# Performance work log

Hardware: AMD Instinct MI355X
Metric: run time of the kernel (lower is better)

Reference implementation:

```python
import jax, jax.numpy as jnp
import numpy as np

B, N, E = 32, 128, 16384
NI, NH, NO, NA = 72, 72, 72, 8
C_WEIGHT = 1.0
EPS = 1e-5  # torch BatchNorm1d default eps


def _psi(p):
    return jnp.sign(p) * jnp.log1p(jnp.abs(p))


def _normsq4(p):
    psq = p * p
    return 2.0 * psq[..., 0] - psq.sum(axis=-1)


def _dotsq4(p, q):
    psq = p * q
    return 2.0 * psq[..., 0] - psq.sum(axis=-1)


def _bn_train(z, g, b):
    # BatchNorm1d in training mode over flattened rows (biased variance)
    mu = z.mean(axis=0)
    var = z.var(axis=0)
    return (z - mu) * jax.lax.rsqrt(var + EPS) * g + b


def _seg_sum(data, ids):
    # data: [B,E,D], ids: [B,E] -> [B,N,D]
    return jax.vmap(lambda d, i: jax.ops.segment_sum(d, i, num_segments=N))(data, ids)


def _init(k, fan_in, shape, scale=1.0):
    return jax.random.normal(k, shape, jnp.float32) * (scale / np.sqrt(fan_in))


def setup_inputs() -> dict:
    key = jax.random.key(0)
    ks = jax.random.split(key, 24)
    d_e_in = 2 * NI + 2
    d_h_in = NH + NI + NA
    return {
        "h": jax.random.normal(ks[0], (B, N, NI), jnp.float32),
        "x": jax.random.normal(ks[1], (B, N, 4), jnp.float32),
        "edgei": jax.random.randint(ks[2], (B, E), 0, N, jnp.int32),
        "edgej": jax.random.randint(ks[3], (B, E), 0, N, jnp.int32),
        "node_attr": jax.random.normal(ks[4], (B, N, NA), jnp.float32),
        # phi_e: Linear(no bias) -> BN -> ReLU -> Linear -> ReLU
        "W_e1": _init(ks[5], d_e_in, (d_e_in, NH)),
        "g_e": jnp.ones((NH,), jnp.float32),
        "be_e": jnp.zeros((NH,), jnp.float32),
        "W_e2": _init(ks[6], NH, (NH, NH)),
        "b_e2": jnp.zeros((NH,), jnp.float32),
        # phi_m: Linear -> Sigmoid
        "W_m": _init(ks[7], NH, (NH, 1)),
        "b_m": jnp.zeros((1,), jnp.float32),
        # phi_x: Linear -> ReLU -> Linear(no bias, tiny xavier gain 0.001)
        "W_x1": _init(ks[8], NH, (NH, NH)),
        "b_x1": jnp.zeros((NH,), jnp.float32),
        "W_x2": _init(ks[9], NH, (NH, 1), scale=0.001),
        # phi_h: Linear -> BN -> ReLU -> Linear
        "W_h1": _init(ks[10], d_h_in, (d_h_in, NH)),
        "b_h1": jnp.zeros((NH,), jnp.float32),
        "g_h": jnp.ones((NH,), jnp.float32),
        "be_h": jnp.zeros((NH,), jnp.float32),
        "W_h2": _init(ks[11], NH, (NH, NO)),
        "b_h2": jnp.zeros((NO,), jnp.float32),
    }


def reference(h, x, edgei, edgej, node_attr, W_e1, g_e, be_e, W_e2, b_e2,
              W_m, b_m, W_x1, b_x1, W_x2, W_h1, b_h1, g_h, be_h, W_h2, b_h2):
    ii = edgei[..., None]  # [B,E,1]
    jj = edgej[..., None]
    # minkowski_feats
    xi = jnp.take_along_axis(x, ii, axis=1)  # [B,E,4]
    xj = jnp.take_along_axis(x, jj, axis=1)
    x_diff = xi - xj
    norms = _psi(_normsq4(x_diff))[..., None]  # [B,E,1]
    dots = _psi(_dotsq4(xi, xj))[..., None]
    # m_model
    hi = jnp.take_along_axis(h, ii, axis=1)  # [B,E,NI]
    hj = jnp.take_along_axis(h, jj, axis=1)
    feat = jnp.concatenate([hi, hj, norms, dots], axis=-1).reshape(-1, 2 * NI + 2)
    z = jax.nn.relu(_bn_train(feat @ W_e1, g_e, be_e))
    z = jax.nn.relu(z @ W_e2 + b_e2)
    m_e = z.reshape(B, E, NH)
    w = jax.nn.sigmoid(m_e @ W_m + b_m)  # [B,E,1]
    m = m_e * w
    # x_model (not last_layer)
    phix = jax.nn.relu(m @ W_x1 + b_x1) @ W_x2  # [B,E,1]
    trans = jnp.clip(x_diff * phix, -100.0, 100.0)
    agg = _seg_sum(trans, edgei)
    cnt = _seg_sum(jnp.ones_like(trans), edgei)
    x_out = x + (agg / jnp.maximum(cnt, 1.0)) * C_WEIGHT
    # h_model
    magg = _seg_sum(m, edgei)  # [B,N,NH]
    cat = jnp.concatenate([h, magg, node_attr], axis=-1).reshape(-1, NH + NI + NA)
    zh = jax.nn.relu(_bn_train(cat @ W_h1 + b_h1, g_h, be_h))
    zh = zh @ W_h2 + b_h2
    h_out = h + zh.reshape(B, N, NO)
    return (h_out, x_out, m)
```

## Files before the change

### kernel.cpp

```cpp
#include <hip/hip_runtime.h>
#include <math.h>

#define B_ 32
#define N_ 128
#define E_ 16384
#define EPS_ 1e-5f

typedef short short8v __attribute__((ext_vector_type(8)));
typedef float f32x4v __attribute__((ext_vector_type(4)));

#define FADD(p, v) unsafeAtomicAdd((p), (v))

#define WS_MAGG    4608
#define WS_AGG     299520
#define WS_CNT     315904
#define WS_ZERO_END 320000
#define WS_AE      320000
#define WS_BE      320072
#define WS_AH      320144
#define WS_BH      320216
#define WS_ZH1     325472
#define WS_PERM    325472
#define WS_HIST    587616
#define WS_OFFS    591712
#define WS_CURS    595808

#define HOUT_OFF 0
#define XOUT_OFF 294912
#define M_OFF    311296

#define NSTAT_T 147456

static __device__ __forceinline__ short f2bf(float f) {
    unsigned int u = __builtin_bit_cast(unsigned int, f);
    u += 0x7FFFu + ((u >> 16) & 1u);
    return (short)(u >> 16);
}

__global__ __launch_bounds__(256) void k_nodeproj(
    const float* __restrict__ h, const float* __restrict__ We1,
    float* __restrict__ Ptop, float* __restrict__ Pmid)
{
    int blk = blockIdx.x;
    int rowBlk = blk >> 3, sub = blk & 7;
    int which = sub >> 2, q = sub & 3;
    int row = rowBlk * 256 + threadIdx.x;
    int c0 = q * 18;
    const float4* h4 = (const float4*)(h + (size_t)row * 72);
    const float* base = We1 + which * 5184 + c0;
    float acc[18];
#pragma unroll
    for (int c = 0; c < 18; ++c) acc[c] = 0.f;
    for (int kc = 0; kc < 18; ++kc) {
        float4 a = h4[kc];
        const float* wr = base + (kc * 4) * 72;
#pragma unroll
        for (int c = 0; c < 18; ++c)
            acc[c] = fmaf(a.x, wr[c], fmaf(a.y, wr[72 + c], fmaf(a.z, wr[144 + c], fmaf(a.w, wr[216 + c], acc[c]))));
    }
    float* P = (which ? Pmid : Ptop) + (size_t)row * 72 + c0;
#pragma unroll
    for (int c = 0; c < 18; ++c) P[c] = acc[c];
}

__global__ __launch_bounds__(256) void k_edge1v3(
    const float* __restrict__ x,
    const int* __restrict__ ei, const int* __restrict__ ej,
    const float* __restrict__ Ptop, const float* __restrict__ Pmid,
    const float* __restrict__ We1,
    float* __restrict__ z1)
{
    int eg = blockIdx.x * 256 + threadIdx.x;
    int b = eg >> 14;
    int i = ei[eg], j = ej[eg];
    int ri = b * N_ + i, rj = b * N_ + j;

    float4 xi = *(const float4*)(x + ri * 4);
    float4 xj = *(const float4*)(x + rj * 4);
    float xdx = xi.x - xj.x, xdy = xi.y - xj.y, xdz = xi.z - xj.z, xdw = xi.w - xj.w;
    float nsq = xdx * xdx - xdy * xdy - xdz * xdz - xdw * xdw;
    float dsq = xi.x * xj.x - xi.y * xj.y - xi.z * xj.z - xi.w * xj.w;
    float norms = copysignf(log1pf(fabsf(nsq)), nsq);
    float dots  = copysignf(log1pf(fabsf(dsq)), dsq);

    const float4* pt4 = (const float4*)(Ptop + (size_t)ri * 72);
    const float4* pm4 = (const float4*)(Pmid + (size_t)rj * 72);
    const float* w144 = We1 + 144 * 72;
    const float* w145 = We1 + 145 * 72;
    float4* zr = (float4*)(z1 + (size_t)eg * 72);

#pragma unroll
    for (int kc = 0; kc < 18; ++kc) {
        float4 a = pt4[kc];
        float4 bq = pm4[kc];
        float4 wa = *(const float4*)(w144 + 4 * kc);
        float4 wb = *(const float4*)(w145 + 4 * kc);
        float4 r;
        r.x = fmaf(norms, wa.x, fmaf(dots, wb.x, a.x + bq.x));
        r.y = fmaf(norms, wa.y, fmaf(dots, wb.y, a.y + bq.y));
        r.z = fmaf(norms, wa.z, fmaf(dots, wb.z, a.z + bq.z));
        r.w = fmaf(norms, wa.w, fmaf(dots, wb.w, a.w + bq.w));
        zr[kc] = r;
    }
}

__global__ __launch_bounds__(256) void k_hist(
    const int* __restrict__ ei, int* __restrict__ hist)
{
    __shared__ int lh[128];
    int t = threadIdx.x;
    if (t < 128) lh[t] = 0;
    __syncthreads();
    int eg = blockIdx.x * 256 + t;
    int b = eg >> 14;
    atomicAdd(&lh[ei[eg]], 1);
    __syncthreads();
    if (t < 128) {
        int v = lh[t];
        if (v) atomicAdd(&hist[b * N_ + t], v);
    }
}

__global__ void k_scan(const int* __restrict__ hist, int* __restrict__ offs,
                       int* __restrict__ curs, float* __restrict__ cnt)
{
    __shared__ int sh[128];
    int b = blockIdx.x, n = threadIdx.x;
    int cv = hist[b * N_ + n];
    sh[n] = cv;
    __syncthreads();
    for (int off = 1; off < 128; off <<= 1) {
        int v = (n >= off) ? sh[n - off] : 0;
        __syncthreads();
        sh[n] += v;
        __syncthreads();
    }
    int excl = sh[n] - cv;
    offs[b * N_ + n] = excl;
    curs[b * N_ + n] = excl;
    cnt[b * N_ + n] = (float)cv;
}

__global__ __launch_bounds__(256) void k_scatter(
    const int* __restrict__ ei, int* __restrict__ curs,
    unsigned short* __restrict__ perm)
{
    int eg = blockIdx.x * 256 + threadIdx.x;
    int b = eg >> 14;
    int i = ei[eg];
    int pos = atomicAdd(&curs[b * N_ + i], 1);
    perm[(size_t)b * E_ + pos] = (unsigned short)(eg & (E_ - 1));
}

__global__ __launch_bounds__(256) void k_stats(
    const float* __restrict__ src, float* __restrict__ sPart,
    float* __restrict__ qPart, int iters)
{
    int tid = blockIdx.x * 256 + threadIdx.x;
    float s0 = 0.f, s1 = 0.f, s2 = 0.f, s3 = 0.f;
    float q0 = 0.f, q1 = 0.f, q2 = 0.f, q3 = 0.f;
    size_t idx = tid;
    const size_t st = NSTAT_T;
    int it = 0;
    for (; it + 3 < iters; it += 4, idx += 4 * st) {
        float v0 = src[idx];
        float v1 = src[idx + st];
        float v2 = src[idx + 2 * st];
        float v3 = src[idx + 3 * st];
        s0 += v0; q0 = fmaf(v0, v0, q0);
        s1 += v1; q1 = fmaf(v1, v1, q1);
        s2 += v2; q2 = fmaf(v2, v2, q2);
        s3 += v3; q3 = fmaf(v3, v3, q3);
    }
    for (; it < iters; ++it, idx += st) {
        float v = src[idx];
        s0 += v; q0 = fmaf(v, v, q0);
    }
    sPart[tid] = (s0 + s1) + (s2 + s3);
    qPart[tid] = (q0 + q1) + (q2 + q3);
}

__global__ __launch_bounds__(256) void k_red(
    const float* __restrict__ sPart, const float* __restrict__ qPart,
    float* __restrict__ sRed, float* __restrict__ qRed)
{
    int tid = blockIdx.x * 256 + threadIdx.x;
    if (tid >= 4608) return;
    int g = tid / 72, c = tid - g * 72;
    int k0 = g * 32;
    float s0 = 0.f, s1 = 0.f, q0 = 0.f, q1 = 0.f;
#pragma unroll 4
    for (int k = 0; k < 32; k += 2) {
        s0 += sPart[c + 72 * (k0 + k)];
        s1 += sPart[c + 72 * (k0 + k + 1)];
        q0 += qPart[c + 72 * (k0 + k)];
        q1 += qPart[c + 72 * (k0 + k + 1)];
    }
    sRed[c + 72 * g] = s0 + s1;
    qRed[c + 72 * g] = q0 + q1;
}

__global__ void k_fin2c(const float* __restrict__ sRed, const float* __restrict__ qRed,
                        const float* __restrict__ g, const float* __restrict__ be,
                        float* __restrict__ A, float* __restrict__ Bv, float Minv)
{
    __shared__ float ss[288], qs[288];
    int t = threadIdx.x;
    int c = t % 72, qq = t / 72;
    float s = 0.f, q = 0.f;
    for (int k = qq; k < 64; k += 4) {
        s += sRed[c + 72 * k];
        q += qRed[c + 72 * k];
    }
    ss[t] = s; qs[t] = q;
    __syncthreads();
    if (t < 72) {
        s = ss[t] + ss[t + 72] + ss[t + 144] + ss[t + 216];
        q = qs[t] + qs[t + 72] + qs[t + 144] + qs[t + 216];
        float mu = s * Minv;
        float var = q * Minv - mu * mu;
        float inv = rsqrtf(var + EPS_);
        float a = g[t] * inv;
        A[t] = a;
        Bv[t] = be[t] - mu * a;
    }
}

__global__ __launch_bounds__(256) void k_e2a(
    const float* __restrict__ We2, const float* __restrict__ be2,
    const float* __restrict__ Wm, const float* __restrict__ bm,
    const float* __restrict__ Ae, const float* __restrict__ Be,
    float* mz)
{
    __shared__ short WtS[80 * 104];
    int t = threadIdx.x;
    for (int idx = t; idx < 80 * 104; idx += 256) {
        int n = idx / 104, k = idx - n * 104;
        float v = (n < 72 && k < 72) ? We2[k * 72 + n] : 0.f;
        WtS[idx] = f2bf(v);
    }
    __syncthreads();

    int base = blockIdx.x * 256;
    int w = t >> 6, l = t & 63, ln = l & 15, g4 = l >> 4;
    float bm0 = bm[0];

    float4 a00 = *(const float4*)(Ae + g4 * 8),      a01 = *(const float4*)(Ae + g4 * 8 + 4);
    float4 b00 = *(const float4*)(Be + g4 * 8),      b01 = *(const float4*)(Be + g4 * 8 + 4);
    float4 a10 = *(const float4*)(Ae + 32 + g4 * 8), a11 = *(const float4*)(Ae + 32 + g4 * 8 + 4);
    float4 b10 = *(const float4*)(Be + 32 + g4 * 8), b11 = *(const float4*)(Be + 32 + g4 * 8 + 4);
    float4 a20, a21, b20, b21;
    if (g4 == 0) {
        a20 = *(const float4*)(Ae + 64); a21 = *(const float4*)(Ae + 68);
        b20 = *(const float4*)(Be + 64); b21 = *(const float4*)(Be + 68);
    } else {
        a20 = make_float4(0, 0, 0, 0); a21 = a20; b20 = a20; b21 = a20;
    }
    float be2v[5], wmv[5];
#pragma unroll
    for (int nt = 0; nt < 5; ++nt) {
        int chan = nt * 16 + ln;
        bool cv = chan < 72;
        be2v[nt] = cv ? be2[chan] : 0.f;
        wmv[nt]  = cv ? Wm[chan]  : 0.f;
    }
    const short8v zero8 = {0, 0, 0, 0, 0, 0, 0, 0};

    for (int ts = 0; ts < 4; ++ts) {
        int es = base + w * 64 + ts * 16;
        const float* zrow = mz + (size_t)(es + ln) * 72 + g4 * 8;
        float4 c0a = *(const float4*)(zrow);
        float4 c0b = *(const float4*)(zrow + 4);
        float4 c1a = *(const float4*)(zrow + 32);
        float4 c1b = *(const float4*)(zrow + 36);

        short8v az0, az1, az2 = zero8;
        az0[0] = f2bf(fmaxf(fmaf(c0a.x, a00.x, b00.x), 0.f));
        az0[1] = f2bf(fmaxf(fmaf(c0a.y, a00.y, b00.y), 0.f));
        az0[2] = f2bf(fmaxf(fmaf(c0a.z, a00.z, b00.z), 0.f));
        az0[3] = f2bf(fmaxf(fmaf(c0a.w, a00.w, b00.w), 0.f));
        az0[4] = f2bf(fmaxf(fmaf(c0b.x, a01.x, b01.x), 0.f));
        az0[5] = f2bf(fmaxf(fmaf(c0b.y, a01.y, b01.y), 0.f));
        az0[6] = f2bf(fmaxf(fmaf(c0b.z, a01.z, b01.z), 0.f));
        az0[7] = f2bf(fmaxf(fmaf(c0b.w, a01.w, b01.w), 0.f));
        az1[0] = f2bf(fmaxf(fmaf(c1a.x, a10.x, b10.x), 0.f));
        az1[1] = f2bf(fmaxf(fmaf(c1a.y, a10.y, b10.y), 0.f));
        az1[2] = f2bf(fmaxf(fmaf(c1a.z, a10.z, b10.z), 0.f));
        az1[3] = f2bf(fmaxf(fmaf(c1a.w, a10.w, b10.w), 0.f));
        az1[4] = f2bf(fmaxf(fmaf(c1b.x, a11.x, b11.x), 0.f));
        az1[5] = f2bf(fmaxf(fmaf(c1b.y, a11.y, b11.y), 0.f));
        az1[6] = f2bf(fmaxf(fmaf(c1b.z, a11.z, b11.z), 0.f));
        az1[7] = f2bf(fmaxf(fmaf(c1b.w, a11.w, b11.w), 0.f));
        if (g4 == 0) {
            float4 c2a = *(const float4*)(mz + (size_t)(es + ln) * 72 + 64);
            float4 c2b = *(const float4*)(mz + (size_t)(es + ln) * 72 + 68);
            az2[0] = f2bf(fmaxf(fmaf(c2a.x, a20.x, b20.x), 0.f));
            az2[1] = f2bf(fmaxf(fmaf(c2a.y, a20.y, b20.y), 0.f));
            az2[2] = f2bf(fmaxf(fmaf(c2a.z, a20.z, b20.z), 0.f));
            az2[3] = f2bf(fmaxf(fmaf(c2a.w, a20.w, b20.w), 0.f));
            az2[4] = f2bf(fmaxf(fmaf(c2b.x, a21.x, b21.x), 0.f));
            az2[5] = f2bf(fmaxf(fmaf(c2b.y, a21.y, b21.y), 0.f));
            az2[6] = f2bf(fmaxf(fmaf(c2b.z, a21.z, b21.z), 0.f));
            az2[7] = f2bf(fmaxf(fmaf(c2b.w, a21.w, b21.w), 0.f));
        }

        f32x4v acc[5];
#pragma unroll
        for (int nt = 0; nt < 5; ++nt) { f32x4v zz = {0.f, 0.f, 0.f, 0.f}; acc[nt] = zz; }
#pragma unroll
        for (int nt = 0; nt < 5; ++nt) {
            int rb = (nt * 16 + ln) * 104 + g4 * 8;
            short8v bw0 = *(const short8v*)&WtS[rb];
            short8v bw1 = *(const short8v*)&WtS[rb + 32];
            short8v bw2 = *(const short8v*)&WtS[rb + 64];
            acc[nt] = __builtin_amdgcn_mfma_f32_16x16x32_bf16(az0, bw0, acc[nt], 0, 0, 0);
            acc[nt] = __builtin_amdgcn_mfma_f32_16x16x32_bf16(az1, bw1, acc[nt], 0, 0, 0);
            acc[nt] = __builtin_amdgcn_mfma_f32_16x16x32_bf16(az2, bw2, acc[nt], 0, 0, 0);
        }

        float mt[5][4];
        float wdot[4] = {bm0, bm0, bm0, bm0};
#pragma unroll
        for (int nt = 0; nt < 5; ++nt) {
#pragma unroll
            for (int r = 0; r < 4; ++r) {
                mt[nt][r] = fmaxf(acc[nt][r] + be2v[nt], 0.f);
                wdot[r] = fmaf(mt[nt][r], wmv[nt], wdot[r]);
            }
        }
#pragma unroll
        for (int r = 0; r < 4; ++r) {
            wdot[r] += __shfl_xor(wdot[r], 1);
            wdot[r] += __shfl_xor(wdot[r], 2);
            wdot[r] += __shfl_xor(wdot[r], 4);
            wdot[r] += __shfl_xor(wdot[r], 8);
            wdot[r] = 1.f / (1.f + expf(-wdot[r]));
        }
#pragma unroll
        for (int nt = 0; nt < 5; ++nt) {
            int chan = nt * 16 + ln;
            if (chan < 72) {
#pragma unroll
                for (int r = 0; r < 4; ++r)
                    mz[(size_t)(es + g4 * 4 + r) * 72 + chan] = mt[nt][r] * wdot[r];
            }
        }
    }
}

__global__ __launch_bounds__(256) void k_e2b(
    const float* __restrict__ x,
    const int* __restrict__ ei, const int* __restrict__ ej,
    const float* __restrict__ bx1, const float* __restrict__ Wx1,
    const float* __restrict__ Wx2,
    const float* mz,
    float* __restrict__ agg)
{
    __shared__ short WtS[80 * 104];
    __shared__ float lagg[128 * 5];
    int t = threadIdx.x;
    for (int idx = t; idx < 128 * 5; idx += 256) lagg[idx] = 0.f;
    for (int idx = t; idx < 80 * 104; idx += 256) {
        int n = idx / 104, k = idx - n * 104;
        float v = (n < 72 && k < 72) ? Wx1[k * 72 + n] : 0.f;
        WtS[idx] = f2bf(v);
    }
    __syncthreads();

    int base = blockIdx.x * 256;
    int b = base >> 14;
    int w = t >> 6, l = t & 63, ln = l & 15, g4 = l >> 4;

    float bxv[5], wxv[5];
#pragma unroll
    for (int nt = 0; nt < 5; ++nt) {
        int chan = nt * 16 + ln;
        bool cv = chan < 72;
        bxv[nt]  = cv ? bx1[chan] : 0.f;
        wxv[nt]  = cv ? Wx2[chan] : 0.f;
    }
    const short8v zero8 = {0, 0, 0, 0, 0, 0, 0, 0};

    for (int ts = 0; ts < 4; ++ts) {
        int es = base + w * 64 + ts * 16;
        const float* mrow = mz + (size_t)(es + ln) * 72 + g4 * 8;
        float4 m0a = *(const float4*)(mrow);
        float4 m0b = *(const float4*)(mrow + 4);
        float4 m1a = *(const float4*)(mrow + 32);
        float4 m1b = *(const float4*)(mrow + 36);

        short8v am0, am1, am2 = zero8;
        am0[0] = f2bf(m0a.x); am0[1] = f2bf(m0a.y); am0[2] = f2bf(m0a.z); am0[3] = f2bf(m0a.w);
        am0[4] = f2bf(m0b.x); am0[5] = f2bf(m0b.y); am0[6] = f2bf(m0b.z); am0[7] = f2bf(m0b.w);
        am1[0] = f2bf(m1a.x); am1[1] = f2bf(m1a.y); am1[2] = f2bf(m1a.z); am1[3] = f2bf(m1a.w);
        am1[4] = f2bf(m1b.x); am1[5] = f2bf(m1b.y); am1[6] = f2bf(m1b.z); am1[7] = f2bf(m1b.w);
        if (g4 == 0) {
            float4 m2a = *(const float4*)(mz + (size_t)(es + ln) * 72 + 64);
            float4 m2b = *(const float4*)(mz + (size_t)(es + ln) * 72 + 68);
            am2[0] = f2bf(m2a.x); am2[1] = f2bf(m2a.y); am2[2] = f2bf(m2a.z); am2[3] = f2bf(m2a.w);
            am2[4] = f2bf(m2b.x); am2[5] = f2bf(m2b.y); am2[6] = f2bf(m2b.z); am2[7] = f2bf(m2b.w);
        }

        f32x4v acc[5];
#pragma unroll
        for (int nt = 0; nt < 5; ++nt) { f32x4v zz = {0.f, 0.f, 0.f, 0.f}; acc[nt] = zz; }
#pragma unroll
        for (int nt = 0; nt < 5; ++nt) {
            int rb = (nt * 16 + ln) * 104 + g4 * 8;
            short8v bw0 = *(const short8v*)&WtS[rb];
            short8v bw1 = *(const short8v*)&WtS[rb + 32];
            short8v bw2 = *(const short8v*)&WtS[rb + 64];
            acc[nt] = __builtin_amdgcn_mfma_f32_16x16x32_bf16(am0, bw0, acc[nt], 0, 0, 0);
            acc[nt] = __builtin_amdgcn_mfma_f32_16x16x32_bf16(am1, bw1, acc[nt], 0, 0, 0);
            acc[nt] = __builtin_amdgcn_mfma_f32_16x16x32_bf16(am2, bw2, acc[nt], 0, 0, 0);
        }

        float ph[4] = {0.f, 0.f, 0.f, 0.f};
#pragma unroll
        for (int nt = 0; nt < 5; ++nt) {
#pragma unroll
            for (int r = 0; r < 4; ++r)
                ph[r] = fmaf(fmaxf(acc[nt][r] + bxv[nt], 0.f), wxv[nt], ph[r]);
        }
#pragma unroll
        for (int r = 0; r < 4; ++r) {
            ph[r] += __shfl_xor(ph[r], 1);
            ph[r] += __shfl_xor(ph[r], 2);
            ph[r] += __shfl_xor(ph[r], 4);
            ph[r] += __shfl_xor(ph[r], 8);
        }
        if (ln == 0) {
#pragma unroll
            for (int r = 0; r < 4; ++r) {
                int eg = es + g4 * 4 + r;
                int ii = ei[eg], jj = ej[eg];
                float4 xi = *(const float4*)(x + (size_t)(b * N_ + ii) * 4);
                float4 xj = *(const float4*)(x + (size_t)(b * N_ + jj) * 4);
                float phx = ph[r];
                float trx = fminf(fmaxf((xi.x - xj.x) * phx, -100.f), 100.f);
                float try_ = fminf(fmaxf((xi.y - xj.y) * phx, -100.f), 100.f);
                float trz = fminf(fmaxf((xi.z - xj.z) * phx, -100.f), 100.f);
                float trw = fminf(fmaxf((xi.w - xj.w) * phx, -100.f), 100.f);
                FADD(&lagg[ii * 5 + 0], trx);
                FADD(&lagg[ii * 5 + 1], try_);
                FADD(&lagg[ii * 5 + 2], trz);
                FADD(&lagg[ii * 5 + 3], trw);
            }
        }
    }
    __syncthreads();

    int nb = b * N_;
    for (int idx = t; idx < 128 * 4; idx += 256) {
        int n = idx >> 2, d = idx & 3;
        float v = lagg[n * 5 + d];
        if (v != 0.f) FADD(&agg[(nb + n) * 4 + d], v);
    }
}

__global__ __launch_bounds__(256) void k_seg2(
    const float* __restrict__ m, const unsigned short* __restrict__ perm,
    const int* __restrict__ offs, const int* __restrict__ hist,
    float* __restrict__ magg)
{
    int tid = blockIdx.x * 256 + threadIdx.x;
    int g = tid / 72, c = tid - g * 72;
    int b = g >> 7;
    int start = offs[g];
    int count = hist[g];
    const unsigned short* p = perm + (size_t)b * E_ + start;
    const float* mb = m + (size_t)b * E_ * 72 + c;
    float a0 = 0.f, a1 = 0.f;
    int k = 0;
    for (; k + 1 < count; k += 2) {
        int e0 = p[k], e1 = p[k + 1];
        a0 += mb[(size_t)e0 * 72];
        a1 += mb[(size_t)e1 * 72];
    }
    if (k < count) a0 += mb[(size_t)p[k] * 72];
    magg[(size_t)g * 72 + c] = a0 + a1;
}

__global__ __launch_bounds__(256) void k_node1v3(
    const float* __restrict__ h, const float* __restrict__ magg,
    const float* __restrict__ attr, const float* __restrict__ Wh1,
    const float* __restrict__ bh1, float* __restrict__ zh1)
{
    int blk = blockIdx.x;
    int q = blk >> 4;
    int row = (blk & 15) * 256 + threadIdx.x;
    int c0 = q * 9;
    float acc[9];
#pragma unroll
    for (int c = 0; c < 9; ++c) acc[c] = bh1[c0 + c];

    const float4* h4 = (const float4*)(h + (size_t)row * 72);
    for (int kc = 0; kc < 18; ++kc) {
        float4 a = h4[kc];
        const float* wr = Wh1 + (kc * 4) * 72 + c0;
#pragma unroll
        for (int c = 0; c < 9; ++c)
            acc[c] = fmaf(a.x, wr[c], fmaf(a.y, wr[72 + c], fmaf(a.z, wr[144 + c], fmaf(a.w, wr[216 + c], acc[c]))));
    }
    const float4* mg4 = (const float4*)(magg + (size_t)row * 72);
    for (int kc = 0; kc < 18; ++kc) {
        float4 a = mg4[kc];
        const float* wr = Wh1 + (72 + kc * 4) * 72 + c0;
#pragma unroll
        for (int c = 0; c < 9; ++c)
            acc[c] = fmaf(a.x, wr[c], fmaf(a.y, wr[72 + c], fmaf(a.z, wr[144 + c], fmaf(a.w, wr[216 + c], acc[c]))));
    }
    const float4* at4 = (const float4*)(attr + (size_t)row * 8);
    for (int kc = 0; kc < 2; ++kc) {
        float4 a = at4[kc];
        const float* wr = Wh1 + (144 + kc * 4) * 72 + c0;
#pragma unroll
        for (int c = 0; c < 9; ++c)
            acc[c] = fmaf(a.x, wr[c], fmaf(a.y, wr[72 + c], fmaf(a.z, wr[144 + c], fmaf(a.w, wr[216 + c], acc[c]))));
    }
    float* zr = zh1 + (size_t)row * 72 + c0;
#pragma unroll
    for (int c = 0; c < 9; ++c) zr[c] = acc[c];
}

__global__ __launch_bounds__(256) void k_node2v2(
    const float* __restrict__ h, const float* __restrict__ x,
    const float* __restrict__ zh1,
    const float* __restrict__ Ah, const float* __restrict__ Bh,
    const float* __restrict__ Wh2, const float* __restrict__ bh2,
    const float* __restrict__ agg, const float* __restrict__ cnt,
    float* __restrict__ hout, float* __restrict__ xout)
{
    int blk = blockIdx.x;
    int q = blk >> 4;
    int row = (blk & 15) * 256 + threadIdx.x;
    int c0 = q * 9;
    float acc[9];
#pragma unroll
    for (int c = 0; c < 9; ++c) acc[c] = bh2[c0 + c];

    const float4* z4 = (const float4*)(zh1 + (size_t)row * 72);
    for (int kc = 0; kc < 18; ++kc) {
        float4 v = z4[kc];
        int k0 = kc * 4;
        float z0 = fmaxf(fmaf(v.x, Ah[k0],     Bh[k0]),     0.f);
        float z1v = fmaxf(fmaf(v.y, Ah[k0 + 1], Bh[k0 + 1]), 0.f);
        float z2v = fmaxf(fmaf(v.z, Ah[k0 + 2], Bh[k0 + 2]), 0.f);
        float z3v = fmaxf(fmaf(v.w, Ah[k0 + 3], Bh[k0 + 3]), 0.f);
        const float* w0 = Wh2 + k0 * 72 + c0;
#pragma unroll
        for (int c = 0; c < 9; ++c)
            acc[c] = fmaf(z0, w0[c], fmaf(z1v, w0[72 + c], fmaf(z2v, w0[144 + c], fmaf(z3v, w0[216 + c], acc[c]))));
    }
    const float* hr = h + (size_t)row * 72 + c0;
    float* ho = hout + (size_t)row * 72 + c0;
#pragma unroll
    for (int c = 0; c < 9; ++c) ho[c] = hr[c] + acc[c];

    if (q == 0) {
        float inv = 1.f / fmaxf(cnt[row], 1.f);
        float4 xv = *(const float4*)(x + (size_t)row * 4);
        float4 av = *(const float4*)(agg + (size_t)row * 4);
        *(float4*)(xout + (size_t)row * 4) = make_float4(xv.x + av.x * inv, xv.y + av.y * inv,
                                                         xv.z + av.z * inv, xv.w + av.w * inv);
    }
}

extern "C" void kernel_launch(void* const* d_in, const int* in_sizes, int n_in,
                              void* d_out, int out_size, void* d_ws, size_t ws_size,
                              hipStream_t stream) {
    const float* h    = (const float*)d_in[0];
    const float* x    = (const float*)d_in[1];
    const int*   ei   = (const int*)d_in[2];
    const int*   ej   = (const int*)d_in[3];
    const float* attr = (const float*)d_in[4];
    const float* We1  = (const float*)d_in[5];
    const float* ge   = (const float*)d_in[6];
    const float* bee  = (const float*)d_in[7];
    const float* We2  = (const float*)d_in[8];
    const float* be2  = (const float*)d_in[9];
    const float* Wm   = (const float*)d_in[10];
    const float* bm   = (const float*)d_in[11];
    const float* Wx1  = (const float*)d_in[12];
    const float* bx1  = (const float*)d_in[13];
    const float* Wx2  = (const float*)d_in[14];
    const float* Wh1  = (const float*)d_in[15];
    const float* bh1  = (const float*)d_in[16];
    const float* gh   = (const float*)d_in[17];
    const float* beh  = (const float*)d_in[18];
    const float* Wh2  = (const float*)d_in[19];
    const float* bh2  = (const float*)d_in[20];

    float* out  = (float*)d_out;
    float* hout = out + HOUT_OFF;
    float* xout = out + XOUT_OFF;
    float* mz   = out + M_OFF;
    float* ws   = (float*)d_ws;
    float* sRed = xout;
    float* qRed = xout + 4608;

    hipMemsetAsync(ws, 0, (size_t)WS_ZERO_END * 4, stream);
    k_nodeproj<<<128, 256, 0, stream>>>(h, We1, ws + WS_ZH1, ws + WS_MAGG);
    k_edge1v3<<<2048, 256, 0, stream>>>(x, ei, ej, ws + WS_ZH1, ws + WS_MAGG, We1, mz);
    hipMemsetAsync(ws + WS_HIST, 0, 4096 * 4, stream);
    k_hist<<<2048, 256, 0, stream>>>(ei, (int*)(ws + WS_HIST));
    k_scan<<<32, 128, 0, stream>>>((const int*)(ws + WS_HIST), (int*)(ws + WS_OFFS),
                                   (int*)(ws + WS_CURS), ws + WS_CNT);
    k_scatter<<<2048, 256, 0, stream>>>(ei, (int*)(ws + WS_CURS),
                                        (unsigned short*)(ws + WS_PERM));
    k_stats<<<576, 256, 0, stream>>>(mz, ws + WS_MAGG, ws + WS_MAGG + NSTAT_T, 256);
    k_red<<<18, 256, 0, stream>>>(ws + WS_MAGG, ws + WS_MAGG + NSTAT_T, sRed, qRed);
    k_fin2c<<<1, 288, 0, stream>>>(sRed, qRed, ge, bee,
                                   ws + WS_AE, ws + WS_BE, 1.0f / (float)(B_ * E_));
    k_e2a<<<2048, 256, 0, stream>>>(We2, be2, Wm, bm, ws + WS_AE, ws + WS_BE, mz);
    k_e2b<<<2048, 256, 0, stream>>>(x, ei, ej, bx1, Wx1, Wx2, mz, ws + WS_AGG);
    k_seg2<<<1152, 256, 0, stream>>>(mz, (const unsigned short*)(ws + WS_PERM),
                                     (const int*)(ws + WS_OFFS), (const int*)(ws + WS_HIST),
                                     ws + WS_MAGG);
    k_node1v3<<<128, 256, 0, stream>>>(h, ws + WS_MAGG, attr, Wh1, bh1, ws + WS_ZH1);
    k_stats<<<576, 256, 0, stream>>>(ws + WS_ZH1, hout, hout + NSTAT_T, 2);
    k_red<<<18, 256, 0, stream>>>(hout, hout + NSTAT_T, sRed, qRed);
    k_fin2c<<<1, 288, 0, stream>>>(sRed, qRed, gh, beh,
                                   ws + WS_AH, ws + WS_BH, 1.0f / 4096.0f);
    k_node2v2<<<128, 256, 0, stream>>>(h, x, ws + WS_ZH1, ws + WS_AH, ws + WS_BH, Wh2, bh2,
                                       ws + WS_AGG, ws + WS_CNT, hout, xout);
}
```

Measured before the change: 389.3 us.

## Fuse edge MLP stage and x-model stage into one kernel via LDS handoff

Merges the two edge kernels (phi_e second layer with sigmoid gate, and phi_x MLP with coordinate aggregation) into one kernel. The gated message is staged as bf16 in shared memory and fed straight into the Wx1 MFMA, so the x-model no longer re-reads the full message tensor from global memory. This also removes one kernel launch. In exchange, shared memory per block grows, which may lower occupancy, and block-wide barriers are now placed inside the tile loop.

```diff
diff --git a/kernel.cpp b/kernel.cpp
--- a/kernel.cpp
+++ b/kernel.cpp
@@ -226,22 +226,32 @@
     }
 }
 
-__global__ __launch_bounds__(256) void k_e2a(
+__global__ __launch_bounds__(256) void k_e2f(
+    const float* __restrict__ x,
+    const int* __restrict__ ei, const int* __restrict__ ej,
     const float* __restrict__ We2, const float* __restrict__ be2,
     const float* __restrict__ Wm, const float* __restrict__ bm,
+    const float* __restrict__ bx1, const float* __restrict__ Wx1,
+    const float* __restrict__ Wx2,
     const float* __restrict__ Ae, const float* __restrict__ Be,
-    float* mz)
-{
-    __shared__ short WtS[80 * 104];
+    float* mz, float* __restrict__ agg)
+{
+    __shared__ short W2S[80 * 104];
+    __shared__ short WxS[80 * 104];
+    __shared__ short mS[4][16 * 80];
+    __shared__ float lagg[128 * 5];
     int t = threadIdx.x;
+    for (int idx = t; idx < 128 * 5; idx += 256) lagg[idx] = 0.f;
     for (int idx = t; idx < 80 * 104; idx += 256) {
         int n = idx / 104, k = idx - n * 104;
-        float v = (n < 72 && k < 72) ? We2[k * 72 + n] : 0.f;
-        WtS[idx] = f2bf(v);
+        bool v = (n < 72 && k < 72);
+        W2S[idx] = f2bf(v ? We2[k * 72 + n] : 0.f);
+        WxS[idx] = f2bf(v ? Wx1[k * 72 + n] : 0.f);
     }
     __syncthreads();
 
     int base = blockIdx.x * 256;
+    int b = base >> 14;
     int w = t >> 6, l = t & 63, ln = l & 15, g4 = l >> 4;
     float bm0 = bm[0];
 
@@ -256,13 +266,15 @@
     } else {
         a20 = make_float4(0, 0, 0, 0); a21 = a20; b20 = a20; b21 = a20;
     }
-    float be2v[5], wmv[5];
+    float be2v[5], wmv[5], bxv[5], wxv[5];
 #pragma unroll
     for (int nt = 0; nt < 5; ++nt) {
         int chan = nt * 16 + ln;
         bool cv = chan < 72;
         be2v[nt] = cv ? be2[chan] : 0.f;
         wmv[nt]  = cv ? Wm[chan]  : 0.f;
+        bxv[nt]  = cv ? bx1[chan] : 0.f;
+        wxv[nt]  = cv ? Wx2[chan] : 0.f;
     }
     const short8v zero8 = {0, 0, 0, 0, 0, 0, 0, 0};
 
@@ -310,9 +322,9 @@
 #pragma unroll
         for (int nt = 0; nt < 5; ++nt) {
             int rb = (nt * 16 + ln) * 104 + g4 * 8;
-            short8v bw0 = *(const short8v*)&WtS[rb];
-            short8v bw1 = *(const short8v*)&WtS[rb + 32];
-            short8v bw2 = *(const short8v*)&WtS[rb + 64];
+            short8v bw0 = *(const short8v*)&W2S[rb];
+            short8v bw1 = *(const short8v*)&W2S[rb + 32];
+            short8v bw2 = *(const short8v*)&W2S[rb + 64];
             acc[nt] = __builtin_amdgcn_mfma_f32_16x16x32_bf16(az0, bw0, acc[nt], 0, 0, 0);
             acc[nt] = __builtin_amdgcn_mfma_f32_16x16x32_bf16(az1, bw1, acc[nt], 0, 0, 0);
             acc[nt] = __builtin_amdgcn_mfma_f32_16x16x32_bf16(az2, bw2, acc[nt], 0, 0, 0);
@@ -339,80 +351,33 @@
 #pragma unroll
         for (int nt = 0; nt < 5; ++nt) {
             int chan = nt * 16 + ln;
-            if (chan < 72) {
-#pragma unroll
-                for (int r = 0; r < 4; ++r)
-                    mz[(size_t)(es + g4 * 4 + r) * 72 + chan] = mt[nt][r] * wdot[r];
+#pragma unroll
+            for (int r = 0; r < 4; ++r) {
+                float mv = mt[nt][r] * wdot[r];
+                mS[w][(g4 * 4 + r) * 80 + chan] = f2bf(mv);
+                if (chan < 72)
+                    mz[(size_t)(es + g4 * 4 + r) * 72 + chan] = mv;
             }
         }
-    }
-}
-
-__global__ __launch_bounds__(256) void k_e2b(
-    const float* __restrict__ x,
-    const int* __restrict__ ei, const int* __restrict__ ej,
-    const float* __restrict__ bx1, const float* __restrict__ Wx1,
-    const float* __restrict__ Wx2,
-    const float* mz,
-    float* __restrict__ agg)
-{
-    __shared__ short WtS[80 * 104];
-    __shared__ float lagg[128 * 5];
-    int t = threadIdx.x;
-    for (int idx = t; idx < 128 * 5; idx += 256) lagg[idx] = 0.f;
-    for (int idx = t; idx < 80 * 104; idx += 256) {
-        int n = idx / 104, k = idx - n * 104;
-        float v = (n < 72 && k < 72) ? Wx1[k * 72 + n] : 0.f;
-        WtS[idx] = f2bf(v);
-    }
-    __syncthreads();
-
-    int base = blockIdx.x * 256;
-    int b = base >> 14;
-    int w = t >> 6, l = t & 63, ln = l & 15, g4 = l >> 4;
-
-    float bxv[5], wxv[5];
-#pragma unroll
-    for (int nt = 0; nt < 5; ++nt) {
-        int chan = nt * 16 + ln;
-        bool cv = chan < 72;
-        bxv[nt]  = cv ? bx1[chan] : 0.f;
-        wxv[nt]  = cv ? Wx2[chan] : 0.f;
-    }
-    const short8v zero8 = {0, 0, 0, 0, 0, 0, 0, 0};
-
-    for (int ts = 0; ts < 4; ++ts) {
-        int es = base + w * 64 + ts * 16;
-        const float* mrow = mz + (size_t)(es + ln) * 72 + g4 * 8;
-        float4 m0a = *(const float4*)(mrow);
-        float4 m0b = *(const float4*)(mrow + 4);
-        float4 m1a = *(const float4*)(mrow + 32);
-        float4 m1b = *(const float4*)(mrow + 36);
-
-        short8v am0, am1, am2 = zero8;
-        am0[0] = f2bf(m0a.x); am0[1] = f2bf(m0a.y); am0[2] = f2bf(m0a.z); am0[3] = f2bf(m0a.w);
-        am0[4] = f2bf(m0b.x); am0[5] = f2bf(m0b.y); am0[6] = f2bf(m0b.z); am0[7] = f2bf(m0b.w);
-        am1[0] = f2bf(m1a.x); am1[1] = f2bf(m1a.y); am1[2] = f2bf(m1a.z); am1[3] = f2bf(m1a.w);
-        am1[4] = f2bf(m1b.x); am1[5] = f2bf(m1b.y); am1[6] = f2bf(m1b.z); am1[7] = f2bf(m1b.w);
-        if (g4 == 0) {
-            float4 m2a = *(const float4*)(mz + (size_t)(es + ln) * 72 + 64);
-            float4 m2b = *(const float4*)(mz + (size_t)(es + ln) * 72 + 68);
-            am2[0] = f2bf(m2a.x); am2[1] = f2bf(m2a.y); am2[2] = f2bf(m2a.z); am2[3] = f2bf(m2a.w);
-            am2[4] = f2bf(m2b.x); am2[5] = f2bf(m2b.y); am2[6] = f2bf(m2b.z); am2[7] = f2bf(m2b.w);
-        }
-
-        f32x4v acc[5];
-#pragma unroll
-        for (int nt = 0; nt < 5; ++nt) { f32x4v zz = {0.f, 0.f, 0.f, 0.f}; acc[nt] = zz; }
+        __syncthreads();
+
+        short8v am0 = *(const short8v*)&mS[w][ln * 80 + g4 * 8];
+        short8v am1 = *(const short8v*)&mS[w][ln * 80 + 32 + g4 * 8];
+        short8v am2 = zero8;
+        if (g4 == 0) am2 = *(const short8v*)&mS[w][ln * 80 + 64];
+
+        f32x4v acc3[5];
+#pragma unroll
+        for (int nt = 0; nt < 5; ++nt) { f32x4v zz = {0.f, 0.f, 0.f, 0.f}; acc3[nt] = zz; }
 #pragma unroll
         for (int nt = 0; nt < 5; ++nt) {
             int rb = (nt * 16 + ln) * 104 + g4 * 8;
-            short8v bw0 = *(const short8v*)&WtS[rb];
-            short8v bw1 = *(const short8v*)&WtS[rb + 32];
-            short8v bw2 = *(const short8v*)&WtS[rb + 64];
-            acc[nt] = __builtin_amdgcn_mfma_f32_16x16x32_bf16(am0, bw0, acc[nt], 0, 0, 0);
-            acc[nt] = __builtin_amdgcn_mfma_f32_16x16x32_bf16(am1, bw1, acc[nt], 0, 0, 0);
-            acc[nt] = __builtin_amdgcn_mfma_f32_16x16x32_bf16(am2, bw2, acc[nt], 0, 0, 0);
+            short8v bw0 = *(const short8v*)&WxS[rb];
+            short8v bw1 = *(const short8v*)&WxS[rb + 32];
+            short8v bw2 = *(const short8v*)&WxS[rb + 64];
+            acc3[nt] = __builtin_amdgcn_mfma_f32_16x16x32_bf16(am0, bw0, acc3[nt], 0, 0, 0);
+            acc3[nt] = __builtin_amdgcn_mfma_f32_16x16x32_bf16(am1, bw1, acc3[nt], 0, 0, 0);
+            acc3[nt] = __builtin_amdgcn_mfma_f32_16x16x32_bf16(am2, bw2, acc3[nt], 0, 0, 0);
         }
 
         float ph[4] = {0.f, 0.f, 0.f, 0.f};
@@ -420,7 +385,7 @@
         for (int nt = 0; nt < 5; ++nt) {
 #pragma unroll
             for (int r = 0; r < 4; ++r)
-                ph[r] = fmaf(fmaxf(acc[nt][r] + bxv[nt], 0.f), wxv[nt], ph[r]);
+                ph[r] = fmaf(fmaxf(acc3[nt][r] + bxv[nt], 0.f), wxv[nt], ph[r]);
         }
 #pragma unroll
         for (int r = 0; r < 4; ++r) {
@@ -447,8 +412,8 @@
                 FADD(&lagg[ii * 5 + 3], trw);
             }
         }
-    }
-    __syncthreads();
+        __syncthreads();
+    }
 
     int nb = b * N_;
     for (int idx = t; idx < 128 * 4; idx += 256) {
@@ -612,8 +577,8 @@
     k_red<<<18, 256, 0, stream>>>(ws + WS_MAGG, ws + WS_MAGG + NSTAT_T, sRed, qRed);
     k_fin2c<<<1, 288, 0, stream>>>(sRed, qRed, ge, bee,
                                    ws + WS_AE, ws + WS_BE, 1.0f / (float)(B_ * E_));
-    k_e2a<<<2048, 256, 0, stream>>>(We2, be2, Wm, bm, ws + WS_AE, ws + WS_BE, mz);
-    k_e2b<<<2048, 256, 0, stream>>>(x, ei, ej, bx1, Wx1, Wx2, mz, ws + WS_AGG);
+    k_e2f<<<2048, 256, 0, stream>>>(x, ei, ej, We2, be2, Wm, bm, bx1, Wx1, Wx2,
+                                    ws + WS_AE, ws + WS_BE, mz, ws + WS_AGG);
     k_seg2<<<1152, 256, 0, stream>>>(mz, (const unsigned short*)(ws + WS_PERM),
                                      (const int*)(ws + WS_OFFS), (const int*)(ws + WS_HIST),
                                      ws + WS_MAGG);
```

Result: faster. 363.0 us (-6.8%).
